# Kernel tuning notes

Hardware: AMD Instinct MI355X
Metric: run time of the kernel (lower is better)

## Reference

```python
import jax, jax.numpy as jnp
import numpy as np

B, K, D = 32768, 4096, 512

def setup_inputs() -> dict:
    key = jax.random.key(0)
    kx, kc = jax.random.split(key)
    x = jax.random.normal(kx, (B, D), dtype=jnp.float32)
    centroids = jax.random.normal(kc, (K, D), dtype=jnp.float32)
    return {"x": x, "centroids": centroids}

def reference(x, centroids):
    # argmin_k ||x_b - c_k||^2. Expand the squared distance so the
    # contraction is a single GEMM instead of a [B,K,D] broadcast:
    xc = x @ centroids.T                      # [B, K]
    c_sq = jnp.sum(centroids * centroids, axis=1)  # [K]
    dists = c_sq[None, :] - 2.0 * xc          # [B, K] (shifted sq-dist)
    action_idcs = jnp.argmin(dists, axis=1)   # [B] int
    return action_idcs
```

## Files before the change

### kernel.cpp

```cpp
#include <hip/hip_runtime.h>
#include <math.h>

#define NB 32768
#define KC 4096
#define DD 512
#define DELTA 2.0f

typedef __attribute__((ext_vector_type(8))) short short8;
typedef __attribute__((ext_vector_type(4))) float facc4;

#define AS1 __attribute__((address_space(1)))
#define AS3 __attribute__((address_space(3)))

__device__ __forceinline__ void gll16(const void* g, void* lds) {
    __builtin_amdgcn_global_load_lds((const AS1 unsigned*)g, (AS3 unsigned*)lds,
                                     16, 0, 0);
}

__device__ __forceinline__ unsigned short f2bf(float f) {
    unsigned u = __float_as_uint(f);
    u += 0x7FFFu + ((u >> 16) & 1u);
    return (unsigned short)(u >> 16);
}
__device__ __forceinline__ unsigned ordenc(float f) {
    unsigned u = __float_as_uint(f);
    return (u & 0x80000000u) ? ~u : (u | 0x80000000u);
}
__device__ __forceinline__ float orddec(unsigned o) {
    unsigned u = (o & 0x80000000u) ? (o & 0x7FFFFFFFu) : ~o;
    return __uint_as_float(u);
}
__device__ __forceinline__ unsigned bf16dn(float f) {
    unsigned u = __float_as_uint(f);
    unsigned t = u >> 16;
    if ((u & 0xFFFFu) && (u >> 31)) t += 1;
    return t & 0xFFFFu;
}
__device__ __forceinline__ float bf16dec(unsigned t) {
    return __uint_as_float(t << 16);
}

__global__ __launch_bounds__(256) void tile_bf16_kernel(const float* __restrict__ in,
                                                        unsigned short* __restrict__ out) {
    const size_t t = (size_t)blockIdx.x * 256 + threadIdx.x;
    const int row = (int)(t >> 6);
    const int d0  = (int)(t & 63) << 3;
    const int blk = row >> 7, r = row & 127;
    const int ks  = d0 >> 5,  dw = d0 & 31;
    const int g   = dw >> 3;
    const int dws = ((g ^ ((r >> 1) & 3)) << 3);
    const float4* p = (const float4*)(in + (size_t)row * DD + d0);
    float4 a = p[0], b = p[1];
    unsigned q0 = (unsigned)f2bf(a.x) | ((unsigned)f2bf(a.y) << 16);
    unsigned q1 = (unsigned)f2bf(a.z) | ((unsigned)f2bf(a.w) << 16);
    unsigned q2 = (unsigned)f2bf(b.x) | ((unsigned)f2bf(b.y) << 16);
    unsigned q3 = (unsigned)f2bf(b.z) | ((unsigned)f2bf(b.w) << 16);
    const size_t o = (((size_t)blk * 16 + ks) * 128 + r) * 32 + dws;
    *(uint4*)(out + o) = make_uint4(q0, q1, q2, q3);
}

__global__ __launch_bounds__(256) void csq_kernel(const float* __restrict__ cent,
                                                  float* __restrict__ csq) {
    const int wid  = threadIdx.x >> 6;
    const int lane = threadIdx.x & 63;
    const int k = (blockIdx.x << 2) + wid;
    const float* row = cent + (size_t)k * DD;
    float s = 0.f;
#pragma unroll
    for (int d = 0; d < DD; d += 64) {
        float v = row[d + lane];
        s = fmaf(v, v, s);
    }
#pragma unroll
    for (int off = 32; off > 0; off >>= 1) s += __shfl_xor(s, off, 64);
    if (lane == 0) csq[k] = s;
}

__global__ __launch_bounds__(256) void gemm_min(
    const unsigned short* __restrict__ xbT, const unsigned short* __restrict__ cbT,
    const float* __restrict__ csq, unsigned long long* __restrict__ locmin64)
{
    __shared__ unsigned short Ab[4096];
    __shared__ unsigned short Bb[4096];

    const int tid = threadIdx.x;
    const int l = tid & 63, w = tid >> 6;
    const int wr = w >> 1, wc = w & 1;

    const int bid = blockIdx.x;
    const int xcd = bid & 7, i = bid >> 3;
    const int mblk = xcd * 32 + (i >> 5);
    const int nblk = i & 31;
    const int m0 = mblk * 128, n0 = nblk * 128;

    const unsigned short* ga = xbT + (size_t)mblk * 16 * 4096 + w * 1024 + l * 8;
    const unsigned short* gb = cbT + (size_t)nblk * 16 * 4096 + w * 1024 + l * 8;

    const int hi = l >> 4, ln = l & 15;
    const int ko = (hi ^ ((ln >> 1) & 3)) << 3;

    facc4 acc[4][4];
#pragma unroll
    for (int fr = 0; fr < 4; ++fr)
#pragma unroll
        for (int fc = 0; fc < 4; ++fc) {
            facc4 z = {0.f, 0.f, 0.f, 0.f};
            acc[fr][fc] = z;
        }

#pragma unroll 1
    for (int ks = 0; ks < 16; ++ks) {
        const unsigned short* sa = ga + (size_t)ks * 4096;
        const unsigned short* sb = gb + (size_t)ks * 4096;
#pragma unroll
        for (int q = 0; q < 2; ++q) {
            gll16(sa + q * 512, &Ab[w * 1024 + q * 512]);
            gll16(sb + q * 512, &Bb[w * 1024 + q * 512]);
        }
        __syncthreads();

        short8 av[4], bv[4];
#pragma unroll
        for (int fr = 0; fr < 4; ++fr)
            av[fr] = *(const short8*)&Ab[(wr * 64 + fr * 16 + ln) * 32 + ko];
#pragma unroll
        for (int fc = 0; fc < 4; ++fc)
            bv[fc] = *(const short8*)&Bb[(wc * 64 + fc * 16 + ln) * 32 + ko];
#pragma unroll
        for (int fr = 0; fr < 4; ++fr)
#pragma unroll
            for (int fc = 0; fc < 4; ++fc)
                acc[fr][fc] = __builtin_amdgcn_mfma_f32_16x16x32_bf16(
                    av[fr], bv[fc], acc[fr][fc], 0, 0, 0);
        __syncthreads();
    }

    const int grp = nblk * 2 + wc;
#pragma unroll
    for (int fr = 0; fr < 4; ++fr) {
#pragma unroll
        for (int j = 0; j < 4; ++j) {
            float m1 = INFINITY, m2 = INFINITY;
            int ix = 0;
#pragma unroll
            for (int fc = 0; fc < 4; ++fc) {
                const float d = fmaf(-2.f, acc[fr][fc][j],
                                     csq[n0 + wc * 64 + fc * 16 + ln]);
                if (d < m1) { m2 = m1; m1 = d; ix = fc * 16 + ln; }
                else        { m2 = fminf(m2, d); }
            }
#pragma unroll
            for (int off = 1; off < 16; off <<= 1) {
                const float om1 = __shfl_xor(m1, off, 64);
                const float om2 = __shfl_xor(m2, off, 64);
                const int   oix = __shfl_xor(ix, off, 64);
                if (om1 < m1) { m2 = fminf(m1, om2); m1 = om1; ix = oix; }
                else          { m2 = fminf(m2, om1); }
            }
            if (ln == 0) {
                const int row = m0 + wr * 64 + fr * 16 + hi * 4 + j;
                const unsigned lo = (bf16dn(m2) << 16) | (unsigned)ix;
                locmin64[(size_t)row * 64 + grp] =
                    ((unsigned long long)ordenc(m1) << 32) | lo;
            }
        }
    }
}

__global__ __launch_bounds__(256) void rescue_argmin_kernel(
    const float* __restrict__ x, const float* __restrict__ cent,
    const float* __restrict__ csq,
    const unsigned long long* __restrict__ locmin64, int* __restrict__ out)
{
    const int row = blockIdx.x * 4 + (threadIdx.x >> 6);
    const int l = threadIdx.x & 63;

    const unsigned long long e = locmin64[(size_t)row * 64 + l];

    unsigned long long v = e;
#pragma unroll
    for (int off = 32; off > 0; off >>= 1) {
        const unsigned long long o = __shfl_xor(v, off, 64);
        v = (o < v) ? o : v;
    }
    const float thr = orddec((unsigned)(v >> 32)) + DELTA;
    unsigned long long qmask = __ballot((unsigned)(e >> 32) <= ordenc(thr));

    const float4* xr = (const float4*)(x + (size_t)row * DD);
    const float4 a0 = xr[l * 2];
    const float4 a1 = xr[l * 2 + 1];

    unsigned long long best = ~0ull;
    while (qmask) {
        const int g = (int)__ffsll((long long)qmask) - 1;
        qmask &= qmask - 1;
        const unsigned long long eg = __shfl(e, g, 64);
        const float m2 = bf16dec((unsigned)(eg >> 16) & 0xFFFFu);
        if (m2 > thr) {
            const int col = g * 64 + (int)(eg & 63u);
            const float4* cr = (const float4*)(cent + (size_t)col * DD);
            const float4 b0 = cr[l * 2], b1 = cr[l * 2 + 1];
            float s = 0.f;
            s = fmaf(a0.x, b0.x, s); s = fmaf(a0.y, b0.y, s);
            s = fmaf(a0.z, b0.z, s); s = fmaf(a0.w, b0.w, s);
            s = fmaf(a1.x, b1.x, s); s = fmaf(a1.y, b1.y, s);
            s = fmaf(a1.z, b1.z, s); s = fmaf(a1.w, b1.w, s);
#pragma unroll
            for (int off = 1; off < 64; off <<= 1) s += __shfl_xor(s, off, 64);
            const float dist = fmaf(-2.f, s, csq[col]);
            const unsigned long long key =
                ((unsigned long long)ordenc(dist) << 32) | (unsigned)col;
            best = (key < best) ? key : best;
        } else {
            const int cl = l >> 1, sg = l & 1;
            const float4* xh = (const float4*)(x + (size_t)row * DD + sg * 256);
            unsigned long long kb = ~0ull;
#pragma unroll
            for (int pass = 0; pass < 2; ++pass) {
                const int col = g * 64 + pass * 32 + cl;
                const float4* ch = (const float4*)(cent + (size_t)col * DD + sg * 256);
                float s0 = 0.f, s1 = 0.f, s2 = 0.f, s3 = 0.f;
#pragma unroll 8
                for (int ee = 0; ee < 64; ++ee) {
                    const float4 a = xh[ee], b = ch[ee];
                    s0 = fmaf(a.x, b.x, s0);
                    s1 = fmaf(a.y, b.y, s1);
                    s2 = fmaf(a.z, b.z, s2);
                    s3 = fmaf(a.w, b.w, s3);
                }
                float s = (s0 + s1) + (s2 + s3);
                s += __shfl_xor(s, 1, 64);
                const float dist = fmaf(-2.f, s, csq[col]);
                const unsigned long long key =
                    ((unsigned long long)ordenc(dist) << 32) | (unsigned)col;
                kb = (key < kb) ? key : kb;
            }
#pragma unroll
            for (int off = 1; off < 64; off <<= 1) {
                const unsigned long long o = __shfl_xor(kb, off, 64);
                kb = (o < kb) ? o : kb;
            }
            best = (kb < best) ? kb : best;
        }
    }
    if (l == 0) out[row] = (int)(best & 0xFFFFFFFFull);
}

__global__ __launch_bounds__(256) void argmin_fp32_kernel(
        const float* __restrict__ x, const float* __restrict__ cent,
        const float* __restrict__ csq, int* __restrict__ out) {
    __shared__ float xs[16][68];
    __shared__ float cs[16][132];
    const int tid = threadIdx.x;
    const int tx = tid & 15;
    const int ty = tid >> 4;
    const int m0 = blockIdx.x * 64;
    const int srow = tid >> 2;
    const int scol = (tid & 3) << 2;
    const float* xg  = x + (size_t)(m0 + srow) * DD + scol;
    const float* cgA = cent + (size_t)srow * DD + scol;
    const float* cgB = cent + (size_t)(srow + 64) * DD + scol;
    float best[4];
    int bidx[4];
#pragma unroll
    for (int i = 0; i < 4; ++i) { best[i] = INFINITY; bidx[i] = 0; }
    for (int n0 = 0; n0 < KC; n0 += 128) {
        float acc[4][2][4];
#pragma unroll
        for (int i = 0; i < 4; ++i)
#pragma unroll
            for (int h = 0; h < 2; ++h)
#pragma unroll
                for (int j = 0; j < 4; ++j) acc[i][h][j] = 0.f;
        const size_t nOff = (size_t)n0 * DD;
        float4 rx = *(const float4*)(xg);
        float4 rc0 = *(const float4*)(cgA + nOff);
        float4 rc1 = *(const float4*)(cgB + nOff);
        for (int k0 = 0; k0 < DD; k0 += 16) {
            __syncthreads();
            const float* p = (const float*)&rx;
            xs[scol + 0][srow] = p[0]; xs[scol + 1][srow] = p[1];
            xs[scol + 2][srow] = p[2]; xs[scol + 3][srow] = p[3];
            const float* q0 = (const float*)&rc0;
            cs[scol + 0][srow] = q0[0]; cs[scol + 1][srow] = q0[1];
            cs[scol + 2][srow] = q0[2]; cs[scol + 3][srow] = q0[3];
            const float* q1 = (const float*)&rc1;
            cs[scol + 0][srow + 64] = q1[0]; cs[scol + 1][srow + 64] = q1[1];
            cs[scol + 2][srow + 64] = q1[2]; cs[scol + 3][srow + 64] = q1[3];
            __syncthreads();
            if (k0 + 16 < DD) {
                rx  = *(const float4*)(xg + k0 + 16);
                rc0 = *(const float4*)(cgA + nOff + k0 + 16);
                rc1 = *(const float4*)(cgB + nOff + k0 + 16);
            }
#pragma unroll
            for (int dd = 0; dd < 16; ++dd) {
                float4 av  = *(const float4*)&xs[dd][ty << 2];
                float4 bv0 = *(const float4*)&cs[dd][tx << 2];
                float4 bv1 = *(const float4*)&cs[dd][64 + (tx << 2)];
                const float* a  = (const float*)&av;
                const float* b0 = (const float*)&bv0;
                const float* b1 = (const float*)&bv1;
#pragma unroll
                for (int i = 0; i < 4; ++i)
#pragma unroll
                    for (int j = 0; j < 4; ++j) {
                        acc[i][0][j] = fmaf(a[i], b0[j], acc[i][0][j]);
                        acc[i][1][j] = fmaf(a[i], b1[j], acc[i][1][j]);
                    }
            }
        }
        float4 qv0 = *(const float4*)(csq + n0 + (tx << 2));
        float4 qv1 = *(const float4*)(csq + n0 + 64 + (tx << 2));
        const float* q0 = (const float*)&qv0;
        const float* q1 = (const float*)&qv1;
#pragma unroll
        for (int i = 0; i < 4; ++i)
#pragma unroll
            for (int h = 0; h < 2; ++h)
#pragma unroll
                for (int j = 0; j < 4; ++j) {
                    float qq = (h == 0) ? q0[j] : q1[j];
                    float dist = fmaf(-2.f, acc[i][h][j], qq);
                    int kk = n0 + h * 64 + (tx << 2) + j;
                    if (dist < best[i] || (dist == best[i] && kk < bidx[i])) {
                        best[i] = dist; bidx[i] = kk;
                    }
                }
    }
#pragma unroll
    for (int off = 1; off < 16; off <<= 1)
#pragma unroll
        for (int i = 0; i < 4; ++i) {
            float ov = __shfl_xor(best[i], off, 64);
            int oi = __shfl_xor(bidx[i], off, 64);
            if (ov < best[i] || (ov == best[i] && oi < bidx[i])) {
                best[i] = ov; bidx[i] = oi;
            }
        }
    if (tx == 0)
#pragma unroll
        for (int i = 0; i < 4; ++i) out[m0 + (ty << 2) + i] = bidx[i];
}

extern "C" void kernel_launch(void* const* d_in, const int* in_sizes, int n_in,
                              void* d_out, int out_size, void* d_ws, size_t ws_size,
                              hipStream_t stream) {
    const float* x    = (const float*)d_in[0];
    const float* cent = (const float*)d_in[1];
    int* out = (int*)d_out;

    const size_t xb_bytes     = (size_t)NB * DD * 2;
    const size_t cb_bytes     = (size_t)KC * DD * 2;
    const size_t locmin_bytes = (size_t)NB * 64 * 8;
    const size_t csq_bytes    = (size_t)KC * 4;
    const size_t need = xb_bytes + cb_bytes + locmin_bytes + csq_bytes;

    if (ws_size >= need) {
        char* p = (char*)d_ws;
        unsigned short* xbT = (unsigned short*)p;              p += xb_bytes;
        unsigned short* cbT = (unsigned short*)p;              p += cb_bytes;
        unsigned long long* locmin64 = (unsigned long long*)p; p += locmin_bytes;
        float* csq = (float*)p;

        tile_bf16_kernel<<<NB * DD / 8 / 256, 256, 0, stream>>>(x, xbT);
        tile_bf16_kernel<<<KC * DD / 8 / 256, 256, 0, stream>>>(cent, cbT);
        csq_kernel<<<KC / 4, 256, 0, stream>>>(cent, csq);
        gemm_min<<<(NB / 128) * (KC / 128), 256, 0, stream>>>(xbT, cbT, csq, locmin64);
        rescue_argmin_kernel<<<NB / 4, 256, 0, stream>>>(x, cent, csq, locmin64, out);
    } else {
        float* csq = (float*)d_ws;
        csq_kernel<<<KC / 4, 256, 0, stream>>>(cent, csq);
        argmin_fp32_kernel<<<NB / 64, 256, 0, stream>>>(x, cent, csq, out);
    }
}
```

Before: 265.5 us.

## Keep full A row-block resident in LDS and stream double-buffered centroid tiles

The GEMM grid is reduced to one workgroup per 128-row block of x. Each workgroup loads its whole 128x512 bf16 A tile into LDS once (128 KB, with a new 64-wide swizzled layout) and then loops over all 32 centroid blocks, double-buffering B k-slices with a prefetch and barrier per step. This removes the repeated reloading of A from global/L2 that the old 8192-block grid did for every (m,n) tile. In exchange it uses very large LDS per block (one block per CU), gives only 256 workgroups, and runs a long serial loop per block, which lowers occupancy and latency hiding.

```diff
diff --git a/kernel.cpp b/kernel.cpp
--- a/kernel.cpp
+++ b/kernel.cpp
@@ -40,8 +40,27 @@
     return __uint_as_float(t << 16);
 }
 
-__global__ __launch_bounds__(256) void tile_bf16_kernel(const float* __restrict__ in,
-                                                        unsigned short* __restrict__ out) {
+__global__ __launch_bounds__(256) void tileA_kernel(const float* __restrict__ in,
+                                                    unsigned short* __restrict__ out) {
+    const size_t t = (size_t)blockIdx.x * 256 + threadIdx.x;
+    const int row = (int)(t >> 6);
+    const int d0  = (int)(t & 63) << 3;
+    const int blk = row >> 7, r = row & 127;
+    const int ks  = d0 >> 6,  dw = d0 & 63;
+    const int g   = dw >> 3;
+    const int dws = ((g ^ (r & 7)) << 3);
+    const float4* p = (const float4*)(in + (size_t)row * DD + d0);
+    float4 a = p[0], b = p[1];
+    unsigned q0 = (unsigned)f2bf(a.x) | ((unsigned)f2bf(a.y) << 16);
+    unsigned q1 = (unsigned)f2bf(a.z) | ((unsigned)f2bf(a.w) << 16);
+    unsigned q2 = (unsigned)f2bf(b.x) | ((unsigned)f2bf(b.y) << 16);
+    unsigned q3 = (unsigned)f2bf(b.z) | ((unsigned)f2bf(b.w) << 16);
+    const size_t o = (((size_t)blk * 8 + ks) * 128 + r) * 64 + dws;
+    *(uint4*)(out + o) = make_uint4(q0, q1, q2, q3);
+}
+
+__global__ __launch_bounds__(256) void tileB_kernel(const float* __restrict__ in,
+                                                    unsigned short* __restrict__ out) {
     const size_t t = (size_t)blockIdx.x * 256 + threadIdx.x;
     const int row = (int)(t >> 6);
     const int d0  = (int)(t & 63) << 3;
@@ -80,88 +99,97 @@
     const unsigned short* __restrict__ xbT, const unsigned short* __restrict__ cbT,
     const float* __restrict__ csq, unsigned long long* __restrict__ locmin64)
 {
-    __shared__ unsigned short Ab[4096];
-    __shared__ unsigned short Bb[4096];
+    __shared__ unsigned short Al[65536];
+    __shared__ unsigned short Bl[2][4096];
 
     const int tid = threadIdx.x;
     const int l = tid & 63, w = tid >> 6;
     const int wr = w >> 1, wc = w & 1;
-
-    const int bid = blockIdx.x;
-    const int xcd = bid & 7, i = bid >> 3;
-    const int mblk = xcd * 32 + (i >> 5);
-    const int nblk = i & 31;
-    const int m0 = mblk * 128, n0 = nblk * 128;
-
-    const unsigned short* ga = xbT + (size_t)mblk * 16 * 4096 + w * 1024 + l * 8;
-    const unsigned short* gb = cbT + (size_t)nblk * 16 * 4096 + w * 1024 + l * 8;
+    const int mblk = blockIdx.x;
+    const int m0 = mblk * 128;
 
     const int hi = l >> 4, ln = l & 15;
-    const int ko = (hi ^ ((ln >> 1) & 3)) << 3;
-
-    facc4 acc[4][4];
-#pragma unroll
-    for (int fr = 0; fr < 4; ++fr)
-#pragma unroll
-        for (int fc = 0; fc < 4; ++fc) {
-            facc4 z = {0.f, 0.f, 0.f, 0.f};
-            acc[fr][fc] = z;
+    const int koB = (hi ^ ((ln >> 1) & 3)) << 3;
+
+    {
+        const unsigned short* gb0 = cbT + w * 1024 + l * 8;
+        gll16(gb0,       &Bl[0][w * 1024]);
+        gll16(gb0 + 512, &Bl[0][w * 1024 + 512]);
+        const unsigned short* ga = xbT + (size_t)mblk * 65536 + w * 16384 + l * 8;
+#pragma unroll
+        for (int i = 0; i < 32; ++i)
+            gll16(ga + i * 512, &Al[w * 16384 + i * 512]);
+        asm volatile("s_waitcnt vmcnt(0)\ns_barrier" ::: "memory");
+    }
+
+#pragma unroll 1
+    for (int nb = 0; nb < 32; ++nb) {
+        const int n0 = nb * 128;
+
+        facc4 acc[4][4];
+#pragma unroll
+        for (int fr = 0; fr < 4; ++fr)
+#pragma unroll
+            for (int fc = 0; fc < 4; ++fc) {
+                facc4 z = {0.f, 0.f, 0.f, 0.f};
+                acc[fr][fc] = z;
+            }
+
+#pragma unroll 2
+        for (int k = 0; k < 16; ++k) {
+            const int t  = nb * 16 + k;
+            const int tn = (t + 1) & 511;
+            const unsigned short* gs = cbT + (size_t)tn * 4096 + w * 1024 + l * 8;
+            gll16(gs,       &Bl[(t + 1) & 1][w * 1024]);
+            gll16(gs + 512, &Bl[(t + 1) & 1][w * 1024 + 512]);
+            asm volatile("s_waitcnt vmcnt(2)\ns_barrier" ::: "memory");
+
+            const unsigned short* Ak = Al + (k >> 1) * 8192;
+            const int koA = (((k & 1) * 4 + hi) ^ (ln & 7)) << 3;
+            short8 av[4], bv[4];
+#pragma unroll
+            for (int fr = 0; fr < 4; ++fr)
+                av[fr] = *(const short8*)&Ak[(wr * 64 + fr * 16 + ln) * 64 + koA];
+#pragma unroll
+            for (int fc = 0; fc < 4; ++fc)
+                bv[fc] = *(const short8*)&Bl[t & 1][(wc * 64 + fc * 16 + ln) * 32 + koB];
+#pragma unroll
+            for (int fr = 0; fr < 4; ++fr)
+#pragma unroll
+                for (int fc = 0; fc < 4; ++fc)
+                    acc[fr][fc] = __builtin_amdgcn_mfma_f32_16x16x32_bf16(
+                        av[fr], bv[fc], acc[fr][fc], 0, 0, 0);
+            asm volatile("s_barrier" ::: "memory");
         }
 
-#pragma unroll 1
-    for (int ks = 0; ks < 16; ++ks) {
-        const unsigned short* sa = ga + (size_t)ks * 4096;
-        const unsigned short* sb = gb + (size_t)ks * 4096;
-#pragma unroll
-        for (int q = 0; q < 2; ++q) {
-            gll16(sa + q * 512, &Ab[w * 1024 + q * 512]);
-            gll16(sb + q * 512, &Bb[w * 1024 + q * 512]);
-        }
-        __syncthreads();
-
-        short8 av[4], bv[4];
-#pragma unroll
-        for (int fr = 0; fr < 4; ++fr)
-            av[fr] = *(const short8*)&Ab[(wr * 64 + fr * 16 + ln) * 32 + ko];
-#pragma unroll
-        for (int fc = 0; fc < 4; ++fc)
-            bv[fc] = *(const short8*)&Bb[(wc * 64 + fc * 16 + ln) * 32 + ko];
-#pragma unroll
-        for (int fr = 0; fr < 4; ++fr)
-#pragma unroll
-            for (int fc = 0; fc < 4; ++fc)
-                acc[fr][fc] = __builtin_amdgcn_mfma_f32_16x16x32_bf16(
-                    av[fr], bv[fc], acc[fr][fc], 0, 0, 0);
-        __syncthreads();
-    }
-
-    const int grp = nblk * 2 + wc;
-#pragma unroll
-    for (int fr = 0; fr < 4; ++fr) {
-#pragma unroll
-        for (int j = 0; j < 4; ++j) {
-            float m1 = INFINITY, m2 = INFINITY;
-            int ix = 0;
-#pragma unroll
-            for (int fc = 0; fc < 4; ++fc) {
-                const float d = fmaf(-2.f, acc[fr][fc][j],
-                                     csq[n0 + wc * 64 + fc * 16 + ln]);
-                if (d < m1) { m2 = m1; m1 = d; ix = fc * 16 + ln; }
-                else        { m2 = fminf(m2, d); }
-            }
-#pragma unroll
-            for (int off = 1; off < 16; off <<= 1) {
-                const float om1 = __shfl_xor(m1, off, 64);
-                const float om2 = __shfl_xor(m2, off, 64);
-                const int   oix = __shfl_xor(ix, off, 64);
-                if (om1 < m1) { m2 = fminf(m1, om2); m1 = om1; ix = oix; }
-                else          { m2 = fminf(m2, om1); }
-            }
-            if (ln == 0) {
-                const int row = m0 + wr * 64 + fr * 16 + hi * 4 + j;
-                const unsigned lo = (bf16dn(m2) << 16) | (unsigned)ix;
-                locmin64[(size_t)row * 64 + grp] =
-                    ((unsigned long long)ordenc(m1) << 32) | lo;
+        const int grp = nb * 2 + wc;
+#pragma unroll
+        for (int fr = 0; fr < 4; ++fr) {
+#pragma unroll
+            for (int j = 0; j < 4; ++j) {
+                float m1 = INFINITY, m2 = INFINITY;
+                int ix = 0;
+#pragma unroll
+                for (int fc = 0; fc < 4; ++fc) {
+                    const float d = fmaf(-2.f, acc[fr][fc][j],
+                                         csq[n0 + wc * 64 + fc * 16 + ln]);
+                    if (d < m1) { m2 = m1; m1 = d; ix = fc * 16 + ln; }
+                    else        { m2 = fminf(m2, d); }
+                }
+#pragma unroll
+                for (int off = 1; off < 16; off <<= 1) {
+                    const float om1 = __shfl_xor(m1, off, 64);
+                    const float om2 = __shfl_xor(m2, off, 64);
+                    const int   oix = __shfl_xor(ix, off, 64);
+                    if (om1 < m1) { m2 = fminf(m1, om2); m1 = om1; ix = oix; }
+                    else          { m2 = fminf(m2, om1); }
+                }
+                if (ln == 0) {
+                    const int row = m0 + wr * 64 + fr * 16 + hi * 4 + j;
+                    const unsigned lo = (bf16dn(m2) << 16) | (unsigned)ix;
+                    locmin64[(size_t)row * 64 + grp] =
+                        ((unsigned long long)ordenc(m1) << 32) | lo;
+                }
             }
         }
     }
@@ -363,10 +391,10 @@
         unsigned long long* locmin64 = (unsigned long long*)p; p += locmin_bytes;
         float* csq = (float*)p;
 
-        tile_bf16_kernel<<<NB * DD / 8 / 256, 256, 0, stream>>>(x, xbT);
-        tile_bf16_kernel<<<KC * DD / 8 / 256, 256, 0, stream>>>(cent, cbT);
+        tileA_kernel<<<NB * DD / 8 / 256, 256, 0, stream>>>(x, xbT);
+        tileB_kernel<<<KC * DD / 8 / 256, 256, 0, stream>>>(cent, cbT);
         csq_kernel<<<KC / 4, 256, 0, stream>>>(cent, csq);
-        gemm_min<<<(NB / 128) * (KC / 128), 256, 0, stream>>>(xbT, cbT, csq, locmin64);
+        gemm_min<<<NB / 128, 256, 0, stream>>>(xbT, cbT, csq, locmin64);
         rescue_argmin_kernel<<<NB / 4, 256, 0, stream>>>(x, cent, csq, locmin64, out);
     } else {
         float* csq = (float*)d_ws;
```

Measured after the change: 482.4 us. 1.82x slower.
